# Performance work log

Hardware: AMD Instinct MI355X
Metric: run time of the kernel (lower is better)

## Reference

```python
import jax, jax.numpy as jnp
import numpy as np

NUM_HEADS = 32
HEAD_DIM = 128
NUM_KV_HEADS = 8
SCALE = 0.08838834764831845  # 1/sqrt(128)
T = 2048          # total packed tokens (total_q == total_k in delta branch)
N_SAL = 512       # number of salient rows
NUM_SEQS = 4
EPS = 1e-8
NEG = -1e30


def setup_inputs() -> dict:
    key = jax.random.key(0)
    ks = jax.random.split(key, 5)
    q = jax.random.normal(ks[0], (T, NUM_HEADS, HEAD_DIM), dtype=jnp.float32)
    k = jax.random.normal(ks[1], (T, NUM_KV_HEADS, HEAD_DIM), dtype=jnp.float32)
    v = jax.random.normal(ks[2], (N_SAL, NUM_KV_HEADS, HEAD_DIM), dtype=jnp.float32)
    v_cache = jax.random.normal(ks[3], (T, NUM_KV_HEADS, HEAD_DIM), dtype=jnp.float32)
    c_cache = jax.random.normal(ks[4], (T, NUM_HEADS * HEAD_DIM), dtype=jnp.float32)
    # unique, sorted salient row indices (torch index_copy requires well-defined scatter)
    idx_salient_row = (jnp.arange(N_SAL, dtype=jnp.int64) * (T // N_SAL))
    # 4 equal packed sequences
    cu_seqlens = jnp.array([0, 512, 1024, 1536, 2048], dtype=jnp.int64)
    return {"q": q, "k": k, "v": v, "v_cache": v_cache, "c_cache": c_cache,
            "idx_salient_row": idx_salient_row, "cu_seqlens": cu_seqlens}


def _segment_ids(cu_seqlens, n):
    # seg[i] = which packed sequence row i belongs to (searchsorted right on bounds)
    return jnp.searchsorted(cu_seqlens[1:], jnp.arange(n), side="right")


def _sdpa(q_, k_, v_, seg_q_, seg_k_):
    # GQA: repeat_interleave kv heads to match query heads
    n_rep = q_.shape[1] // k_.shape[1]
    if n_rep > 1:
        k_ = jnp.repeat(k_, n_rep, axis=1)
        v_ = jnp.repeat(v_, n_rep, axis=1)
    scores = jnp.einsum("qhd,khd->hqk", q_, k_) * SCALE  # [H, nq, T]
    allow = (seg_q_[:, None] == seg_k_[None, :])          # [nq, T]
    scores = jnp.where(allow[None, :, :], scores, NEG)
    p = jax.nn.softmax(scores, axis=-1)
    return jnp.einsum("hqk,khd->qhd", p, v_)              # [nq, H, D]


def reference(q, k, v, v_cache, c_cache, idx_salient_row, cu_seqlens):
    total = q.shape[0]
    seg = _segment_ids(cu_seqlens, total)  # seg_q == seg_k (total_q == total_k)

    # delta KV-cache update at salient rows
    v_delta = v - v_cache[idx_salient_row]                      # [n_sal, Hkv, D]
    v_delta_sparse = jnp.zeros_like(k).at[idx_salient_row].set(v_delta)
    v_cache_new = v_cache.at[idx_salient_row].set(v)

    # salient-row full attention against updated cache
    o_salient = _sdpa(q[idx_salient_row], k, v_cache_new, seg[idx_salient_row], seg)
    # sparse delta attention for every row
    delta_c = _sdpa(q, k, v_delta_sparse, seg, seg)

    new_c_flat = c_cache + delta_c.reshape(total, -1)
    new_c_flat = new_c_flat.at[idx_salient_row].set(o_salient.reshape(o_salient.shape[0], -1))

    # cosine similarity between old and new context (early-exit signal)
    num = jnp.sum(c_cache * new_c_flat, axis=-1)
    den_c = jnp.sum(c_cache * c_cache, axis=-1)
    den_n = jnp.sum(new_c_flat * new_c_flat, axis=-1)
    cos_sim = num / (jnp.sqrt(den_c) * jnp.sqrt(den_n) + EPS)

    return new_c_flat.reshape(total, NUM_HEADS, HEAD_DIM), cos_sim
```

## Files before the change

kernel.cpp:

```cpp
#include <hip/hip_runtime.h>
#include <math.h>

#define NUM_HEADS 32
#define HEAD_DIM 128
#define NUM_KV_HEADS 8
#define SCALE 0.08838834764831845f
#define EPS 1e-8f
#define MAX_SEG 512
#define QT 32
#define BLK 512
#define SEGC_MAX 16
#define PB_STRIDE 520
#define TLD 130
#define CD (NUM_HEADS * HEAD_DIM)

typedef __bf16 bf16x8 __attribute__((ext_vector_type(8)));
typedef __bf16 bf16x4 __attribute__((ext_vector_type(4)));
typedef float  f32x4  __attribute__((ext_vector_type(4)));

#define MFMA16(a, b, c) __builtin_amdgcn_mfma_f32_16x16x32_bf16((a), (b), (c), 0, 0, 0)

__device__ __forceinline__ int lower_bound_i(const int* __restrict__ a, int n, int key) {
    int lo = 0, hi = n;
    while (lo < hi) { int mid = (lo + hi) >> 1; if (a[mid] < key) lo = mid + 1; else hi = mid; }
    return lo;
}
__device__ __forceinline__ int bsearch_eq(const int* __restrict__ a, int n, int key) {
    int lo = lower_bound_i(a, n, key);
    return (lo < n && a[lo] == key) ? lo : -1;
}

__device__ __forceinline__ bf16x8 cvt8(const float* p) {
    float4 f0 = *(const float4*)p;
    float4 f1 = *(const float4*)(p + 4);
    bf16x8 a;
    a[0]=(__bf16)f0.x; a[1]=(__bf16)f0.y; a[2]=(__bf16)f0.z; a[3]=(__bf16)f0.w;
    a[4]=(__bf16)f1.x; a[5]=(__bf16)f1.y; a[6]=(__bf16)f1.z; a[7]=(__bf16)f1.w;
    return a;
}

__device__ __forceinline__ void red16(float& xn, float& xc, float& xd) {
#pragma unroll
    for (int m = 1; m <= 8; m <<= 1) {
        xn += __shfl_xor(xn, m, 64);
        xc += __shfl_xor(xc, m, 64);
        xd += __shfl_xor(xd, m, 64);
    }
}

__global__ void prep(const float* __restrict__ k, const float* __restrict__ v,
                     const float* __restrict__ vc, const int* __restrict__ idx,
                     const int* __restrict__ cu,
                     __bf16* __restrict__ kb, __bf16* __restrict__ vnewT,
                     __bf16* __restrict__ vdScat, int* __restrict__ tinfo,
                     int* __restrict__ rowsal,
                     int T, int Tpad, int n_sal, int n_seq,
                     int nb_conv, int nb_vt) {
    __shared__ __bf16 tileN[64 * TLD];
    __shared__ __bf16 tileD[64 * TLD];
    __shared__ int sal_of[64];
    const int b = blockIdx.x;
    const int tid = threadIdx.x;

    if (b < nb_conv) {
        int i = b * 256 + tid;
        int n8 = T * NUM_KV_HEADS * HEAD_DIM / 8;
        if (i < n8) {
            const float4* s4 = (const float4*)(k + (size_t)i * 8);
            float4 a = s4[0], bb = s4[1];
            bf16x8 o;
            o[0]=(__bf16)a.x; o[1]=(__bf16)a.y; o[2]=(__bf16)a.z; o[3]=(__bf16)a.w;
            o[4]=(__bf16)bb.x; o[5]=(__bf16)bb.y; o[6]=(__bf16)bb.z; o[7]=(__bf16)bb.w;
            *(bf16x8*)(kb + (size_t)i * 8) = o;
        }
        return;
    }
    if (b < nb_conv + nb_vt * NUM_KV_HEADS) {
        const int bb = b - nb_conv;
        const int kv = bb / nb_vt;
        const int r0 = (bb % nb_vt) * 64;
        if (tid < 64) sal_of[tid] = bsearch_eq(idx, n_sal, r0 + tid);
        __syncthreads();
        for (int ii = tid; ii < 64 * 32; ii += 256) {
            int r = ii >> 5, c4 = ii & 31;
            int row = r0 + r;
            float4 fN = {0.f, 0.f, 0.f, 0.f};
            float4 fD = {0.f, 0.f, 0.f, 0.f};
            if (row < T) {
                int s2 = sal_of[r];
                if (s2 >= 0) {
                    float4 a  = *(const float4*)(v  + ((size_t)s2  * NUM_KV_HEADS + kv) * HEAD_DIM + c4 * 4);
                    float4 c  = *(const float4*)(vc + ((size_t)row * NUM_KV_HEADS + kv) * HEAD_DIM + c4 * 4);
                    fN = a;
                    fD.x = a.x - c.x; fD.y = a.y - c.y; fD.z = a.z - c.z; fD.w = a.w - c.w;
                } else {
                    fN = *(const float4*)(vc + ((size_t)row * NUM_KV_HEADS + kv) * HEAD_DIM + c4 * 4);
                }
            }
            __bf16* tn = &tileN[r * TLD + c4 * 4];
            tn[0] = (__bf16)fN.x; tn[1] = (__bf16)fN.y; tn[2] = (__bf16)fN.z; tn[3] = (__bf16)fN.w;
            __bf16* td = &tileD[r * TLD + c4 * 4];
            td[0] = (__bf16)fD.x; td[1] = (__bf16)fD.y; td[2] = (__bf16)fD.z; td[3] = (__bf16)fD.w;
        }
        __syncthreads();
        for (int ii = tid; ii < 128 * 8; ii += 256) {
            int d = ii >> 3, rg = ii & 7;
            int row_out = r0 + rg * 8;
            if (row_out < Tpad) {
                bf16x8 oN, oD;
#pragma unroll
                for (int j = 0; j < 8; j++) {
                    oN[j] = tileN[(rg * 8 + j) * TLD + d];
                    oD[j] = tileD[(rg * 8 + j) * TLD + d];
                }
                *(bf16x8*)(vnewT  + ((size_t)kv * HEAD_DIM + d) * Tpad + row_out) = oN;
                *(bf16x8*)(vdScat + ((size_t)kv * HEAD_DIM + d) * Tpad + row_out) = oD;
            }
        }
        return;
    }
    {
        for (int i = tid; i < T; i += 256) rowsal[i] = -1;
        __syncthreads();
        for (int s = tid; s < n_sal; s += 256) rowsal[idx[s]] = s;
        const int NT = T / QT;
        for (int t = tid; t < NT; t += 256) {
            const int r0 = t * QT;
            int a = 0, e = T;
            for (int s = 0; s < n_seq; s++) {
                int x = cu[s], y = cu[s + 1];
                if (r0 >= x && r0 < y) { a = x; e = y; }
            }
            tinfo[t * 4 + 0] = a;
            tinfo[t * 4 + 1] = e;
            tinfo[t * 4 + 2] = 0;
            tinfo[t * 4 + 3] = 0;
        }
    }
}


#define QK_TILE_GEN(ttc) {                                                                  \
    const int t_ = wave * 4 + (ttc);                                                        \
    if (t_ < ntiles) {                                                                      \
        int key_ = seg_start + t_ * 16 + lm;                                                \
        if (key_ >= seg_end) key_ = seg_end - 1;                                            \
        const __bf16* kp_ = kb + ((size_t)key_ * NUM_KV_HEADS + kvh) * HEAD_DIM + quad * 8; \
        const bf16x8 bk0_ = *(const bf16x8*)(kp_);                                          \
        const bf16x8 bk1_ = *(const bf16x8*)(kp_ + 32);                                     \
        const bf16x8 bk2_ = *(const bf16x8*)(kp_ + 64);                                     \
        const bf16x8 bk3_ = *(const bf16x8*)(kp_ + 96);                                     \
        f32x4 a0_ = {0.f,0.f,0.f,0.f}, a1_ = {0.f,0.f,0.f,0.f};                             \
        a0_ = MFMA16(bk0_, aq00, a0_);  a1_ = MFMA16(bk0_, aq10, a1_);                      \
        a0_ = MFMA16(bk1_, aq01, a0_);  a1_ = MFMA16(bk1_, aq11, a1_);                      \
        a0_ = MFMA16(bk2_, aq02, a0_);  a1_ = MFMA16(bk2_, aq12, a1_);                      \
        a0_ = MFMA16(bk3_, aq03, a0_);  a1_ = MFMA16(bk3_, aq13, a1_);                      \
        bf16x4 pk0_, pk1_;                                                                  \
        _Pragma("unroll")                                                                   \
        for (int r_ = 0; r_ < 4; r_++) {                                                    \
            const int kl_ = t_ * 16 + quad * 4 + r_;                                        \
            const bool ok_ = (kl_ < seg_len);                                               \
            float e0_ = ok_ ? __expf(a0_[r_] * SCALE) : 0.f;                                \
            float e1_ = ok_ ? __expf(a1_[r_] * SCALE) : 0.f;                                \
            ps0 += e0_; ps1 += e1_;                                                         \
            pk0_[r_] = (__bf16)e0_; pk1_[r_] = (__bf16)e1_;                                 \
        }                                                                                   \
        *(bf16x4*)&Pb[lm * PB_STRIDE + t_ * 16 + quad * 4] = pk0_;                          \
        *(bf16x4*)&Pb[(16 + lm) * PB_STRIDE + t_ * 16 + quad * 4] = pk1_;                   \
    } }

#define LOADK(buf, t) {                                                                     \
    const __bf16* kn_ = kp + (size_t)(t) * 16 * krow;                                       \
    kk[buf][0] = *(const bf16x8*)(kn_);                                                     \
    kk[buf][1] = *(const bf16x8*)(kn_ + 32);                                                \
    kk[buf][2] = *(const bf16x8*)(kn_ + 64);                                                \
    kk[buf][3] = *(const bf16x8*)(kn_ + 96); }

__global__ __launch_bounds__(BLK, 4)
void attn_mfma(const float* __restrict__ q, const __bf16* __restrict__ kb,
               const __bf16* __restrict__ vnewT, const __bf16* __restrict__ vdScat,
               const float* __restrict__ c_cache, const int* __restrict__ tinfo,
               const int* __restrict__ rowsal,
               float* __restrict__ out_c, float* __restrict__ cospart, int Tpad) {
    const int bid  = blockIdx.x;
    const int kvh  = bid & 7;
    const int rem  = bid >> 3;
    const int h    = kvh * 4 + (rem & 3);
    const int qt   = rem >> 2;
    const int qrow0 = qt * QT;
    const int tid   = threadIdx.x;
    const int wave  = tid >> 6;
    const int lane  = tid & 63;
    const int lm    = lane & 15;
    const int quad  = lane >> 4;

    __shared__ __align__(16) __bf16 Pb[QT * PB_STRIDE];
    __shared__ float wred[8 * QT];
    __shared__ float linv[QT];
    __shared__ int   salrow[QT];
    __shared__ float cp[8 * 3 * QT];

    const int4 ti = *(const int4*)(tinfo + qt * 4);
    const int seg_start = ti.x, seg_end = ti.y;
    const int seg_len = seg_end - seg_start;
    const int ntiles = (seg_len + 15) >> 4;
    const int SEGC   = (seg_len + 31) >> 5;
    const int dim = wave * 16 + lm;

    if (tid < QT) salrow[tid] = rowsal[qrow0 + tid];
    if (ntiles * 16 < SEGC * 32) {
        for (int ii = tid; ii < QT * 16; ii += BLK) {
            int row = ii >> 4, col = ntiles * 16 + (ii & 15);
            Pb[row * PB_STRIDE + col] = (__bf16)0.f;
        }
    }

    bf16x8 aq00, aq01, aq02, aq03, aq10, aq11, aq12, aq13;
    {
        const float* qp0 = q + ((size_t)(qrow0 + lm) * NUM_HEADS + h) * HEAD_DIM + quad * 8;
        const float* qp1 = q + ((size_t)(qrow0 + 16 + lm) * NUM_HEADS + h) * HEAD_DIM + quad * 8;
        aq00 = cvt8(qp0);      aq01 = cvt8(qp0 + 32); aq02 = cvt8(qp0 + 64); aq03 = cvt8(qp0 + 96);
        aq10 = cvt8(qp1);      aq11 = cvt8(qp1 + 32); aq12 = cvt8(qp1 + 64); aq13 = cvt8(qp1 + 96);
    }

    const float* cbase = c_cache + (size_t)qrow0 * CD + h * HEAD_DIM + dim;
    float cold[2][4];
#pragma unroll
    for (int rt = 0; rt < 2; rt++)
#pragma unroll
        for (int r = 0; r < 4; r++)
            cold[rt][r] = cbase[(size_t)(rt * 16 + quad * 4 + r) * CD];

    float ps0 = 0.f, ps1 = 0.f;
    if (seg_len == MAX_SEG) {
        const size_t krow = (size_t)NUM_KV_HEADS * HEAD_DIM;
        const __bf16* kp = kb + (size_t)(seg_start + wave * 64 + lm) * krow
                              + (size_t)kvh * HEAD_DIM + quad * 8;
        bf16x8 kk[3][4];
        LOADK(0, 0)
        LOADK(1, 1)
#pragma unroll
        for (int tt = 0; tt < 4; tt++) {
            if (tt + 2 < 4) LOADK((tt + 2) % 3, tt + 2)
            const int cur = tt % 3;
            f32x4 a0_ = {0.f,0.f,0.f,0.f}, a1_ = {0.f,0.f,0.f,0.f};
            a0_ = MFMA16(kk[cur][0], aq00, a0_);  a1_ = MFMA16(kk[cur][0], aq10, a1_);
            a0_ = MFMA16(kk[cur][1], aq01, a0_);  a1_ = MFMA16(kk[cur][1], aq11, a1_);
            a0_ = MFMA16(kk[cur][2], aq02, a0_);  a1_ = MFMA16(kk[cur][2], aq12, a1_);
            a0_ = MFMA16(kk[cur][3], aq03, a0_);  a1_ = MFMA16(kk[cur][3], aq13, a1_);
            const int t_ = wave * 4 + tt;
            bf16x4 pk0_, pk1_;
#pragma unroll
            for (int r_ = 0; r_ < 4; r_++) {
                float e0_ = __expf(a0_[r_] * SCALE);
                float e1_ = __expf(a1_[r_] * SCALE);
                ps0 += e0_; ps1 += e1_;
                pk0_[r_] = (__bf16)e0_; pk1_[r_] = (__bf16)e1_;
            }
            *(bf16x4*)&Pb[lm * PB_STRIDE + t_ * 16 + quad * 4] = pk0_;
            *(bf16x4*)&Pb[(16 + lm) * PB_STRIDE + t_ * 16 + quad * 4] = pk1_;
        }
    } else {
        QK_TILE_GEN(0) QK_TILE_GEN(1) QK_TILE_GEN(2) QK_TILE_GEN(3)
    }
#pragma unroll
    for (int m = 16; m <= 32; m <<= 1) {
        ps0 += __shfl_xor(ps0, m, 64);
        ps1 += __shfl_xor(ps1, m, 64);
    }
    if (quad == 0) {
        wred[wave * QT + lm]      = ps0;
        wred[wave * QT + 16 + lm] = ps1;
    }

    const __bf16* vF = vnewT  + ((size_t)kvh * HEAD_DIM + dim) * Tpad + seg_start + quad * 8;
    const __bf16* vD = vdScat + ((size_t)kvh * HEAD_DIM + dim) * Tpad + seg_start + quad * 8;
    const __bf16* pb0 = &Pb[lm * PB_STRIDE + quad * 8];
    const __bf16* pb1 = &Pb[(16 + lm) * PB_STRIDE + quad * 8];
    bf16x8 fv[4], dv[4];
#pragma unroll
    for (int i = 0; i < 3; i++) {
        fv[i] = *(const bf16x8*)(vF + i * 32);
        dv[i] = *(const bf16x8*)(vD + i * 32);
    }

    __syncthreads();
    if (tid < QT) {
        float s = 0.f;
#pragma unroll
        for (int w = 0; w < 8; w++) s += wred[w * QT + tid];
        linv[tid] = 1.f / s;
    }

    __builtin_amdgcn_s_setprio(1);
    f32x4 accF0 = {0.f,0.f,0.f,0.f}, accF1 = {0.f,0.f,0.f,0.f};
    f32x4 accD0 = {0.f,0.f,0.f,0.f}, accD1 = {0.f,0.f,0.f,0.f};
    if (SEGC == SEGC_MAX) {
        bf16x8 a0c = *(const bf16x8*)(pb0);
        bf16x8 a1c = *(const bf16x8*)(pb1);
#pragma unroll
        for (int cc = 0; cc < SEGC_MAX; cc++) {
            bf16x8 a0n, a1n;
            if (cc + 1 < SEGC_MAX) {
                a0n = *(const bf16x8*)(pb0 + (cc + 1) * 32);
                a1n = *(const bf16x8*)(pb1 + (cc + 1) * 32);
            }
            if (cc + 3 < SEGC_MAX) {
                fv[(cc + 3) & 3] = *(const bf16x8*)(vF + (cc + 3) * 32);
                dv[(cc + 3) & 3] = *(const bf16x8*)(vD + (cc + 3) * 32);
            }
            const int cur = cc & 3;
            accF0 = MFMA16(a0c, fv[cur], accF0);
            accF1 = MFMA16(a1c, fv[cur], accF1);
            accD0 = MFMA16(a0c, dv[cur], accD0);
            accD1 = MFMA16(a1c, dv[cur], accD1);
            if (cc + 1 < SEGC_MAX) { a0c = a0n; a1c = a1n; }
        }
    } else {
        for (int cc = 0; cc < SEGC; cc++) {
            const bf16x8 bF_ = *(const bf16x8*)(vF + cc * 32);
            const bf16x8 bD_ = *(const bf16x8*)(vD + cc * 32);
            const bf16x8 a0_ = *(const bf16x8*)(pb0 + cc * 32);
            const bf16x8 a1_ = *(const bf16x8*)(pb1 + cc * 32);
            accF0 = MFMA16(a0_, bF_, accF0);
            accF1 = MFMA16(a1_, bF_, accF1);
            accD0 = MFMA16(a0_, bD_, accD0);
            accD1 = MFMA16(a1_, bD_, accD1);
        }
    }
    __builtin_amdgcn_s_setprio(0);
    __syncthreads();

    float* obase = out_c + (size_t)qrow0 * CD + h * HEAD_DIM + dim;
#pragma unroll
    for (int rt = 0; rt < 2; rt++) {
#pragma unroll
        for (int r = 0; r < 4; r++) {
            const int row = rt * 16 + quad * 4 + r;
            const float c_old = cold[rt][r];
            const float li = linv[row];
            const float aF = (rt == 0) ? accF0[r] : accF1[r];
            const float aD = (rt == 0) ? accD0[r] : accD1[r];
            const float o = (salrow[row] >= 0) ? aF * li : c_old + aD * li;
            obase[(size_t)row * CD] = o;
            float xn = o * c_old, xc = c_old * c_old, xd = o * o;
            red16(xn, xc, xd);
            if (lm == 0) {
                cp[(wave * 3 + 0) * QT + row] = xn;
                cp[(wave * 3 + 1) * QT + row] = xc;
                cp[(wave * 3 + 2) * QT + row] = xd;
            }
        }
    }
    __syncthreads();
    for (int ii = tid; ii < 3 * QT; ii += BLK) {
        int c = ii >> 5, row = ii & 31;
        float s = 0.f;
#pragma unroll
        for (int w = 0; w < 8; w++) s += cp[(w * 3 + c) * QT + row];
        cospart[((size_t)(qrow0 + row) * 3 + c) * NUM_HEADS + h] = s;
    }
}

__global__ void cos_finalize(const float* __restrict__ cospart, float* __restrict__ out_cos, int T) {
    const int lane = threadIdx.x & 63;
    const int row  = blockIdx.x * 4 + (threadIdx.x >> 6);
    if (row >= T) return;
    const float* p = cospart + (size_t)row * (NUM_HEADS * 3);
    float a = p[lane];
    float b = (lane < 32) ? p[64 + lane] : 0.f;
#pragma unroll
    for (int m = 1; m <= 16; m <<= 1) {
        a += __shfl_xor(a, m, 64);
        b += __shfl_xor(b, m, 64);
    }
    float den_c = __shfl(a, 32, 64);
    if (lane == 0) out_cos[row] = a / (sqrtf(den_c) * sqrtf(b) + EPS);
}

extern "C" void kernel_launch(void* const* d_in, const int* in_sizes, int n_in,
                              void* d_out, int out_size, void* d_ws, size_t ws_size,
                              hipStream_t stream) {
    const float* q       = (const float*)d_in[0];
    const float* k       = (const float*)d_in[1];
    const float* v       = (const float*)d_in[2];
    const float* v_cache = (const float*)d_in[3];
    const float* c_cache = (const float*)d_in[4];
    const int*   idx     = (const int*)d_in[5];
    const int*   cu      = (const int*)d_in[6];

    const int T     = in_sizes[0] / CD;
    const int n_sal = in_sizes[5];
    const int n_seq = in_sizes[6] - 1;
    const int Tpad  = T + 32;
    const int NT    = T / QT;

    float* out_c   = (float*)d_out;
    float* out_cos = out_c + (size_t)T * CD;

    char* wsp = (char*)d_ws;
    size_t off = 0;
    __bf16* kb = (__bf16*)(wsp + off);
    off += (((size_t)T * NUM_KV_HEADS * HEAD_DIM * 2) + 255) & ~(size_t)255;
    __bf16* vnewT = (__bf16*)(wsp + off);
    off += (((size_t)NUM_KV_HEADS * HEAD_DIM * Tpad * 2) + 255) & ~(size_t)255;
    __bf16* vdScat = (__bf16*)(wsp + off);
    off += (((size_t)NUM_KV_HEADS * HEAD_DIM * Tpad * 2) + 255) & ~(size_t)255;
    float* cospart = (float*)(wsp + off);
    off += ((size_t)T * NUM_HEADS * 3 * 4 + 255) & ~(size_t)255;
    int* tinfo = (int*)(wsp + off);
    off += ((size_t)NT * 4 * 4 + 255) & ~(size_t)255;
    int* rowsal = (int*)(wsp + off);
    off += ((size_t)T * 4 + 255) & ~(size_t)255;
    (void)ws_size;

    const int nb_conv = (T * NUM_KV_HEADS * HEAD_DIM / 8 + 255) / 256;
    const int nb_vt   = (Tpad + 63) / 64;
    const int nb_tot  = nb_conv + nb_vt * NUM_KV_HEADS + 1;

    prep<<<nb_tot, 256, 0, stream>>>(k, v, v_cache, idx, cu, kb, vnewT, vdScat,
                                     tinfo, rowsal, T, Tpad, n_sal, n_seq,
                                     nb_conv, nb_vt);

    attn_mfma<<<NT * NUM_HEADS, BLK, 0, stream>>>(q, kb, vnewT, vdScat, c_cache,
                                                  tinfo, rowsal, out_c, cospart, Tpad);

    cos_finalize<<<(T + 3) / 4, 256, 0, stream>>>(cospart, out_cos, T);
}
```

Before: 227.7 us.

## Process two query heads per block to halve grid size and amortize setup

Each attention block now loops over two query heads that share a KV head, so the grid shrinks from NT*32 to NT*16 blocks. The per-block setup (tile info, salient-row flags, Pb padding) is done once for both heads, and the V tiles may be reused through cache between the two iterations. Cosine partials are accumulated across the two heads in shared memory, and cos_finalize is reworked for the resulting 16-wide partial layout. The cost is fewer blocks, which leaves less parallelism to hide latency, plus the head loop running serially inside each block.

```diff
diff --git a/kernel.cpp b/kernel.cpp
--- a/kernel.cpp
+++ b/kernel.cpp
@@ -184,9 +184,8 @@
                float* __restrict__ out_c, float* __restrict__ cospart, int Tpad) {
     const int bid  = blockIdx.x;
     const int kvh  = bid & 7;
-    const int rem  = bid >> 3;
-    const int h    = kvh * 4 + (rem & 3);
-    const int qt   = rem >> 2;
+    const int sub  = (bid >> 3) & 1;
+    const int qt   = bid >> 4;
     const int qrow0 = qt * QT;
     const int tid   = threadIdx.x;
     const int wave  = tid >> 6;
@@ -215,140 +214,147 @@
         }
     }
 
-    bf16x8 aq00, aq01, aq02, aq03, aq10, aq11, aq12, aq13;
-    {
-        const float* qp0 = q + ((size_t)(qrow0 + lm) * NUM_HEADS + h) * HEAD_DIM + quad * 8;
-        const float* qp1 = q + ((size_t)(qrow0 + 16 + lm) * NUM_HEADS + h) * HEAD_DIM + quad * 8;
-        aq00 = cvt8(qp0);      aq01 = cvt8(qp0 + 32); aq02 = cvt8(qp0 + 64); aq03 = cvt8(qp0 + 96);
-        aq10 = cvt8(qp1);      aq11 = cvt8(qp1 + 32); aq12 = cvt8(qp1 + 64); aq13 = cvt8(qp1 + 96);
-    }
-
-    const float* cbase = c_cache + (size_t)qrow0 * CD + h * HEAD_DIM + dim;
-    float cold[2][4];
-#pragma unroll
-    for (int rt = 0; rt < 2; rt++)
-#pragma unroll
-        for (int r = 0; r < 4; r++)
-            cold[rt][r] = cbase[(size_t)(rt * 16 + quad * 4 + r) * CD];
-
-    float ps0 = 0.f, ps1 = 0.f;
-    if (seg_len == MAX_SEG) {
-        const size_t krow = (size_t)NUM_KV_HEADS * HEAD_DIM;
-        const __bf16* kp = kb + (size_t)(seg_start + wave * 64 + lm) * krow
-                              + (size_t)kvh * HEAD_DIM + quad * 8;
-        bf16x8 kk[3][4];
-        LOADK(0, 0)
-        LOADK(1, 1)
-#pragma unroll
-        for (int tt = 0; tt < 4; tt++) {
-            if (tt + 2 < 4) LOADK((tt + 2) % 3, tt + 2)
-            const int cur = tt % 3;
-            f32x4 a0_ = {0.f,0.f,0.f,0.f}, a1_ = {0.f,0.f,0.f,0.f};
-            a0_ = MFMA16(kk[cur][0], aq00, a0_);  a1_ = MFMA16(kk[cur][0], aq10, a1_);
-            a0_ = MFMA16(kk[cur][1], aq01, a0_);  a1_ = MFMA16(kk[cur][1], aq11, a1_);
-            a0_ = MFMA16(kk[cur][2], aq02, a0_);  a1_ = MFMA16(kk[cur][2], aq12, a1_);
-            a0_ = MFMA16(kk[cur][3], aq03, a0_);  a1_ = MFMA16(kk[cur][3], aq13, a1_);
-            const int t_ = wave * 4 + tt;
-            bf16x4 pk0_, pk1_;
-#pragma unroll
-            for (int r_ = 0; r_ < 4; r_++) {
-                float e0_ = __expf(a0_[r_] * SCALE);
-                float e1_ = __expf(a1_[r_] * SCALE);
-                ps0 += e0_; ps1 += e1_;
-                pk0_[r_] = (__bf16)e0_; pk1_[r_] = (__bf16)e1_;
-            }
-            *(bf16x4*)&Pb[lm * PB_STRIDE + t_ * 16 + quad * 4] = pk0_;
-            *(bf16x4*)&Pb[(16 + lm) * PB_STRIDE + t_ * 16 + quad * 4] = pk1_;
-        }
-    } else {
-        QK_TILE_GEN(0) QK_TILE_GEN(1) QK_TILE_GEN(2) QK_TILE_GEN(3)
-    }
-#pragma unroll
-    for (int m = 16; m <= 32; m <<= 1) {
-        ps0 += __shfl_xor(ps0, m, 64);
-        ps1 += __shfl_xor(ps1, m, 64);
-    }
-    if (quad == 0) {
-        wred[wave * QT + lm]      = ps0;
-        wred[wave * QT + 16 + lm] = ps1;
-    }
-
     const __bf16* vF = vnewT  + ((size_t)kvh * HEAD_DIM + dim) * Tpad + seg_start + quad * 8;
     const __bf16* vD = vdScat + ((size_t)kvh * HEAD_DIM + dim) * Tpad + seg_start + quad * 8;
     const __bf16* pb0 = &Pb[lm * PB_STRIDE + quad * 8];
     const __bf16* pb1 = &Pb[(16 + lm) * PB_STRIDE + quad * 8];
-    bf16x8 fv[4], dv[4];
-#pragma unroll
-    for (int i = 0; i < 3; i++) {
-        fv[i] = *(const bf16x8*)(vF + i * 32);
-        dv[i] = *(const bf16x8*)(vD + i * 32);
-    }
-
-    __syncthreads();
-    if (tid < QT) {
-        float s = 0.f;
-#pragma unroll
-        for (int w = 0; w < 8; w++) s += wred[w * QT + tid];
-        linv[tid] = 1.f / s;
-    }
-
-    __builtin_amdgcn_s_setprio(1);
-    f32x4 accF0 = {0.f,0.f,0.f,0.f}, accF1 = {0.f,0.f,0.f,0.f};
-    f32x4 accD0 = {0.f,0.f,0.f,0.f}, accD1 = {0.f,0.f,0.f,0.f};
-    if (SEGC == SEGC_MAX) {
-        bf16x8 a0c = *(const bf16x8*)(pb0);
-        bf16x8 a1c = *(const bf16x8*)(pb1);
-#pragma unroll
-        for (int cc = 0; cc < SEGC_MAX; cc++) {
-            bf16x8 a0n, a1n;
-            if (cc + 1 < SEGC_MAX) {
-                a0n = *(const bf16x8*)(pb0 + (cc + 1) * 32);
-                a1n = *(const bf16x8*)(pb1 + (cc + 1) * 32);
-            }
-            if (cc + 3 < SEGC_MAX) {
-                fv[(cc + 3) & 3] = *(const bf16x8*)(vF + (cc + 3) * 32);
-                dv[(cc + 3) & 3] = *(const bf16x8*)(vD + (cc + 3) * 32);
-            }
-            const int cur = cc & 3;
-            accF0 = MFMA16(a0c, fv[cur], accF0);
-            accF1 = MFMA16(a1c, fv[cur], accF1);
-            accD0 = MFMA16(a0c, dv[cur], accD0);
-            accD1 = MFMA16(a1c, dv[cur], accD1);
-            if (cc + 1 < SEGC_MAX) { a0c = a0n; a1c = a1n; }
-        }
-    } else {
-        for (int cc = 0; cc < SEGC; cc++) {
-            const bf16x8 bF_ = *(const bf16x8*)(vF + cc * 32);
-            const bf16x8 bD_ = *(const bf16x8*)(vD + cc * 32);
-            const bf16x8 a0_ = *(const bf16x8*)(pb0 + cc * 32);
-            const bf16x8 a1_ = *(const bf16x8*)(pb1 + cc * 32);
-            accF0 = MFMA16(a0_, bF_, accF0);
-            accF1 = MFMA16(a1_, bF_, accF1);
-            accD0 = MFMA16(a0_, bD_, accD0);
-            accD1 = MFMA16(a1_, bD_, accD1);
-        }
-    }
-    __builtin_amdgcn_s_setprio(0);
-    __syncthreads();
-
-    float* obase = out_c + (size_t)qrow0 * CD + h * HEAD_DIM + dim;
-#pragma unroll
-    for (int rt = 0; rt < 2; rt++) {
-#pragma unroll
-        for (int r = 0; r < 4; r++) {
-            const int row = rt * 16 + quad * 4 + r;
-            const float c_old = cold[rt][r];
-            const float li = linv[row];
-            const float aF = (rt == 0) ? accF0[r] : accF1[r];
-            const float aD = (rt == 0) ? accD0[r] : accD1[r];
-            const float o = (salrow[row] >= 0) ? aF * li : c_old + aD * li;
-            obase[(size_t)row * CD] = o;
-            float xn = o * c_old, xc = c_old * c_old, xd = o * o;
-            red16(xn, xc, xd);
-            if (lm == 0) {
-                cp[(wave * 3 + 0) * QT + row] = xn;
-                cp[(wave * 3 + 1) * QT + row] = xc;
-                cp[(wave * 3 + 2) * QT + row] = xd;
+
+#pragma unroll 1
+    for (int u = 0; u < 2; u++) {
+        const int h = kvh * 4 + sub * 2 + u;
+
+        bf16x8 aq00, aq01, aq02, aq03, aq10, aq11, aq12, aq13;
+        {
+            const float* qp0 = q + ((size_t)(qrow0 + lm) * NUM_HEADS + h) * HEAD_DIM + quad * 8;
+            const float* qp1 = q + ((size_t)(qrow0 + 16 + lm) * NUM_HEADS + h) * HEAD_DIM + quad * 8;
+            aq00 = cvt8(qp0);      aq01 = cvt8(qp0 + 32); aq02 = cvt8(qp0 + 64); aq03 = cvt8(qp0 + 96);
+            aq10 = cvt8(qp1);      aq11 = cvt8(qp1 + 32); aq12 = cvt8(qp1 + 64); aq13 = cvt8(qp1 + 96);
+        }
+        const float* cbase = c_cache + (size_t)qrow0 * CD + h * HEAD_DIM + dim;
+        float cold[2][4];
+#pragma unroll
+        for (int rt = 0; rt < 2; rt++)
+#pragma unroll
+            for (int r = 0; r < 4; r++)
+                cold[rt][r] = cbase[(size_t)(rt * 16 + quad * 4 + r) * CD];
+
+        float ps0 = 0.f, ps1 = 0.f;
+        if (seg_len == MAX_SEG) {
+            const size_t krow = (size_t)NUM_KV_HEADS * HEAD_DIM;
+            const __bf16* kp = kb + (size_t)(seg_start + wave * 64 + lm) * krow
+                                  + (size_t)kvh * HEAD_DIM + quad * 8;
+            bf16x8 kk[3][4];
+            LOADK(0, 0)
+            LOADK(1, 1)
+#pragma unroll
+            for (int tt = 0; tt < 4; tt++) {
+                if (tt + 2 < 4) LOADK((tt + 2) % 3, tt + 2)
+                const int cur = tt % 3;
+                f32x4 a0_ = {0.f,0.f,0.f,0.f}, a1_ = {0.f,0.f,0.f,0.f};
+                a0_ = MFMA16(kk[cur][0], aq00, a0_);  a1_ = MFMA16(kk[cur][0], aq10, a1_);
+                a0_ = MFMA16(kk[cur][1], aq01, a0_);  a1_ = MFMA16(kk[cur][1], aq11, a1_);
+                a0_ = MFMA16(kk[cur][2], aq02, a0_);  a1_ = MFMA16(kk[cur][2], aq12, a1_);
+                a0_ = MFMA16(kk[cur][3], aq03, a0_);  a1_ = MFMA16(kk[cur][3], aq13, a1_);
+                const int t_ = wave * 4 + tt;
+                bf16x4 pk0_, pk1_;
+#pragma unroll
+                for (int r_ = 0; r_ < 4; r_++) {
+                    float e0_ = __expf(a0_[r_] * SCALE);
+                    float e1_ = __expf(a1_[r_] * SCALE);
+                    ps0 += e0_; ps1 += e1_;
+                    pk0_[r_] = (__bf16)e0_; pk1_[r_] = (__bf16)e1_;
+                }
+                *(bf16x4*)&Pb[lm * PB_STRIDE + t_ * 16 + quad * 4] = pk0_;
+                *(bf16x4*)&Pb[(16 + lm) * PB_STRIDE + t_ * 16 + quad * 4] = pk1_;
+            }
+        } else {
+            QK_TILE_GEN(0) QK_TILE_GEN(1) QK_TILE_GEN(2) QK_TILE_GEN(3)
+        }
+#pragma unroll
+        for (int m = 16; m <= 32; m <<= 1) {
+            ps0 += __shfl_xor(ps0, m, 64);
+            ps1 += __shfl_xor(ps1, m, 64);
+        }
+        if (quad == 0) {
+            wred[wave * QT + lm]      = ps0;
+            wred[wave * QT + 16 + lm] = ps1;
+        }
+
+        bf16x8 fv[4], dv[4];
+#pragma unroll
+        for (int i = 0; i < 3; i++) {
+            fv[i] = *(const bf16x8*)(vF + i * 32);
+            dv[i] = *(const bf16x8*)(vD + i * 32);
+        }
+
+        __syncthreads();
+        if (tid < QT) {
+            float s = 0.f;
+#pragma unroll
+            for (int w = 0; w < 8; w++) s += wred[w * QT + tid];
+            linv[tid] = 1.f / s;
+        }
+
+        __builtin_amdgcn_s_setprio(1);
+        f32x4 accF0 = {0.f,0.f,0.f,0.f}, accF1 = {0.f,0.f,0.f,0.f};
+        f32x4 accD0 = {0.f,0.f,0.f,0.f}, accD1 = {0.f,0.f,0.f,0.f};
+        if (SEGC == SEGC_MAX) {
+            bf16x8 a0c = *(const bf16x8*)(pb0);
+            bf16x8 a1c = *(const bf16x8*)(pb1);
+#pragma unroll
+            for (int cc = 0; cc < SEGC_MAX; cc++) {
+                bf16x8 a0n, a1n;
+                if (cc + 1 < SEGC_MAX) {
+                    a0n = *(const bf16x8*)(pb0 + (cc + 1) * 32);
+                    a1n = *(const bf16x8*)(pb1 + (cc + 1) * 32);
+                }
+                if (cc + 3 < SEGC_MAX) {
+                    fv[(cc + 3) & 3] = *(const bf16x8*)(vF + (cc + 3) * 32);
+                    dv[(cc + 3) & 3] = *(const bf16x8*)(vD + (cc + 3) * 32);
+                }
+                const int cur = cc & 3;
+                accF0 = MFMA16(a0c, fv[cur], accF0);
+                accF1 = MFMA16(a1c, fv[cur], accF1);
+                accD0 = MFMA16(a0c, dv[cur], accD0);
+                accD1 = MFMA16(a1c, dv[cur], accD1);
+                if (cc + 1 < SEGC_MAX) { a0c = a0n; a1c = a1n; }
+            }
+        } else {
+            for (int cc = 0; cc < SEGC; cc++) {
+                const bf16x8 bF_ = *(const bf16x8*)(vF + cc * 32);
+                const bf16x8 bD_ = *(const bf16x8*)(vD + cc * 32);
+                const bf16x8 a0_ = *(const bf16x8*)(pb0 + cc * 32);
+                const bf16x8 a1_ = *(const bf16x8*)(pb1 + cc * 32);
+                accF0 = MFMA16(a0_, bF_, accF0);
+                accF1 = MFMA16(a1_, bF_, accF1);
+                accD0 = MFMA16(a0_, bD_, accD0);
+                accD1 = MFMA16(a1_, bD_, accD1);
+            }
+        }
+        __builtin_amdgcn_s_setprio(0);
+        __syncthreads();
+
+        float* obase = out_c + (size_t)qrow0 * CD + h * HEAD_DIM + dim;
+#pragma unroll
+        for (int rt = 0; rt < 2; rt++) {
+#pragma unroll
+            for (int r = 0; r < 4; r++) {
+                const int row = rt * 16 + quad * 4 + r;
+                const float c_old = cold[rt][r];
+                const float li = linv[row];
+                const float aF = (rt == 0) ? accF0[r] : accF1[r];
+                const float aD = (rt == 0) ? accD0[r] : accD1[r];
+                const float o = (salrow[row] >= 0) ? aF * li : c_old + aD * li;
+                obase[(size_t)row * CD] = o;
+                float xn = o * c_old, xc = c_old * c_old, xd = o * o;
+                red16(xn, xc, xd);
+                if (lm == 0) {
+                    const int s0 = (wave * 3 + 0) * QT + row;
+                    const int s1 = (wave * 3 + 1) * QT + row;
+                    const int s2 = (wave * 3 + 2) * QT + row;
+                    if (u == 0) { cp[s0] = xn;  cp[s1] = xc;  cp[s2] = xd; }
+                    else        { cp[s0] += xn; cp[s1] += xc; cp[s2] += xd; }
+                }
             }
         }
     }
@@ -358,7 +364,7 @@
         float s = 0.f;
 #pragma unroll
         for (int w = 0; w < 8; w++) s += cp[(w * 3 + c) * QT + row];
-        cospart[((size_t)(qrow0 + row) * 3 + c) * NUM_HEADS + h] = s;
+        cospart[(size_t)(qrow0 + row) * 48 + c * 16 + kvh * 2 + sub] = s;
     }
 }
 
@@ -366,16 +372,16 @@
     const int lane = threadIdx.x & 63;
     const int row  = blockIdx.x * 4 + (threadIdx.x >> 6);
     if (row >= T) return;
-    const float* p = cospart + (size_t)row * (NUM_HEADS * 3);
-    float a = p[lane];
-    float b = (lane < 32) ? p[64 + lane] : 0.f;
-#pragma unroll
-    for (int m = 1; m <= 16; m <<= 1) {
-        a += __shfl_xor(a, m, 64);
-        b += __shfl_xor(b, m, 64);
-    }
-    float den_c = __shfl(a, 32, 64);
-    if (lane == 0) out_cos[row] = a / (sqrtf(den_c) * sqrtf(b) + EPS);
+    const float* p = cospart + (size_t)row * 48;
+    float vv = (lane < 48) ? p[lane] : 0.f;
+    vv += __shfl_xor(vv, 1, 64);
+    vv += __shfl_xor(vv, 2, 64);
+    vv += __shfl_xor(vv, 4, 64);
+    vv += __shfl_xor(vv, 8, 64);
+    const float nn = __shfl(vv, 0, 64);
+    const float dc = __shfl(vv, 16, 64);
+    const float dd = __shfl(vv, 32, 64);
+    if (lane == 0) out_cos[row] = nn / (sqrtf(dc) * sqrtf(dd) + EPS);
 }
 
 extern "C" void kernel_launch(void* const* d_in, const int* in_sizes, int n_in,
@@ -407,7 +413,7 @@
     __bf16* vdScat = (__bf16*)(wsp + off);
     off += (((size_t)NUM_KV_HEADS * HEAD_DIM * Tpad * 2) + 255) & ~(size_t)255;
     float* cospart = (float*)(wsp + off);
-    off += ((size_t)T * NUM_HEADS * 3 * 4 + 255) & ~(size_t)255;
+    off += ((size_t)T * 48 * 4 + 255) & ~(size_t)255;
     int* tinfo = (int*)(wsp + off);
     off += ((size_t)NT * 4 * 4 + 255) & ~(size_t)255;
     int* rowsal = (int*)(wsp + off);
@@ -422,8 +428,8 @@
                                      tinfo, rowsal, T, Tpad, n_sal, n_seq,
                                      nb_conv, nb_vt);
 
-    attn_mfma<<<NT * NUM_HEADS, BLK, 0, stream>>>(q, kb, vnewT, vdScat, c_cache,
-                                                  tinfo, rowsal, out_c, cospart, Tpad);
+    attn_mfma<<<NT * 16, BLK, 0, stream>>>(q, kb, vnewT, vdScat, c_cache,
+                                           tinfo, rowsal, out_c, cospart, Tpad);
 
     cos_finalize<<<(T + 3) / 4, 256, 0, stream>>>(cospart, out_cos, T);
 }
```

New measurement: 311.6 us. 36.9% more time.

## Compact delta attention to salient columns only in PV matmul

Applied to the files above, without the earlier changes.

Adds a compacted, transposed v_delta buffer holding only the salient rows, plus per-tile salient index ranges. The attention kernel scatters the probabilities of salient keys into a small Pd shared tile and runs the delta PV matmul over only those columns, instead of multiplying against the mostly zero dense scattered V delta. This removes about three quarters of the delta MFMAs and V loads. It costs extra shared memory, per-key rowsal lookups during softmax, and extra prep blocks.

```diff
diff --git a/kernel.cpp b/kernel.cpp
--- a/kernel.cpp
+++ b/kernel.cpp
@@ -11,6 +11,10 @@
 #define BLK 512
 #define SEGC_MAX 16
 #define PB_STRIDE 520
+#define PD_STRIDE 136
+#define PD_MAX 128
+#define SAL_PAD 576
+#define SAL_STRIDE 640
 #define TLD 130
 #define CD (NUM_HEADS * HEAD_DIM)
 
@@ -52,10 +56,10 @@
                      const float* __restrict__ vc, const int* __restrict__ idx,
                      const int* __restrict__ cu,
                      __bf16* __restrict__ kb, __bf16* __restrict__ vnewT,
-                     __bf16* __restrict__ vdScat, int* __restrict__ tinfo,
-                     int* __restrict__ rowsal,
+                     __bf16* __restrict__ vdScat, __bf16* __restrict__ vdT,
+                     int* __restrict__ tinfo, int* __restrict__ rowsal,
                      int T, int Tpad, int n_sal, int n_seq,
-                     int nb_conv, int nb_vt) {
+                     int nb_conv, int nb_vt, int nb_vd) {
     __shared__ __bf16 tileN[64 * TLD];
     __shared__ __bf16 tileD[64 * TLD];
     __shared__ int sal_of[64];
@@ -119,6 +123,33 @@
         }
         return;
     }
+    if (b < nb_conv + nb_vt * NUM_KV_HEADS + nb_vd * NUM_KV_HEADS) {
+        const int bb = b - nb_conv - nb_vt * NUM_KV_HEADS;
+        const int kv = bb / nb_vd;
+        const int s0 = (bb % nb_vd) * 64;
+        for (int ii = tid; ii < 64 * 32; ii += 256) {
+            int r = ii >> 5, c4 = ii & 31;
+            int s = s0 + r;
+            float4 f = {0.f, 0.f, 0.f, 0.f};
+            if (s < n_sal) {
+                int row = idx[s];
+                float4 a  = *(const float4*)(v  + ((size_t)s   * NUM_KV_HEADS + kv) * HEAD_DIM + c4 * 4);
+                float4 c2 = *(const float4*)(vc + ((size_t)row * NUM_KV_HEADS + kv) * HEAD_DIM + c4 * 4);
+                f.x = a.x - c2.x; f.y = a.y - c2.y; f.z = a.z - c2.z; f.w = a.w - c2.w;
+            }
+            __bf16* tp = &tileN[r * TLD + c4 * 4];
+            tp[0] = (__bf16)f.x; tp[1] = (__bf16)f.y; tp[2] = (__bf16)f.z; tp[3] = (__bf16)f.w;
+        }
+        __syncthreads();
+        for (int ii = tid; ii < 128 * 8; ii += 256) {
+            int d = ii >> 3, rg = ii & 7;
+            bf16x8 o;
+#pragma unroll
+            for (int j = 0; j < 8; j++) o[j] = tileN[(rg * 8 + j) * TLD + d];
+            *(bf16x8*)(vdT + ((size_t)kv * HEAD_DIM + d) * SAL_STRIDE + s0 + rg * 8) = o;
+        }
+        return;
+    }
     {
         for (int i = tid; i < T; i += 256) rowsal[i] = -1;
         __syncthreads();
@@ -133,8 +164,8 @@
             }
             tinfo[t * 4 + 0] = a;
             tinfo[t * 4 + 1] = e;
-            tinfo[t * 4 + 2] = 0;
-            tinfo[t * 4 + 3] = 0;
+            tinfo[t * 4 + 2] = lower_bound_i(idx, n_sal, a);
+            tinfo[t * 4 + 3] = lower_bound_i(idx, n_sal, e);
         }
     }
 }
@@ -164,6 +195,14 @@
             float e1_ = ok_ ? __expf(a1_[r_] * SCALE) : 0.f;                                \
             ps0 += e0_; ps1 += e1_;                                                         \
             pk0_[r_] = (__bf16)e0_; pk1_[r_] = (__bf16)e1_;                                 \
+            if (compact && ok_) {                                                           \
+                int sr_ = rowsal[seg_start + kl_];                                          \
+                if (sr_ >= 0) {                                                             \
+                    int c_ = sr_ - s_lo;                                                    \
+                    Pd[lm * PD_STRIDE + c_]        = pk0_[r_];                              \
+                    Pd[(16 + lm) * PD_STRIDE + c_] = pk1_[r_];                              \
+                }                                                                           \
+            }                                                                               \
         }                                                                                   \
         *(bf16x4*)&Pb[lm * PB_STRIDE + t_ * 16 + quad * 4] = pk0_;                          \
         *(bf16x4*)&Pb[(16 + lm) * PB_STRIDE + t_ * 16 + quad * 4] = pk1_;                   \
@@ -179,9 +218,11 @@
 __global__ __launch_bounds__(BLK, 4)
 void attn_mfma(const float* __restrict__ q, const __bf16* __restrict__ kb,
                const __bf16* __restrict__ vnewT, const __bf16* __restrict__ vdScat,
+               const __bf16* __restrict__ vdT,
                const float* __restrict__ c_cache, const int* __restrict__ tinfo,
                const int* __restrict__ rowsal,
-               float* __restrict__ out_c, float* __restrict__ cospart, int Tpad) {
+               float* __restrict__ out_c, float* __restrict__ cospart,
+               int Tpad, int use_compact) {
     const int bid  = blockIdx.x;
     const int kvh  = bid & 7;
     const int rem  = bid >> 3;
@@ -195,17 +236,20 @@
     const int quad  = lane >> 4;
 
     __shared__ __align__(16) __bf16 Pb[QT * PB_STRIDE];
+    __shared__ __align__(16) __bf16 Pd[QT * PD_STRIDE];
     __shared__ float wred[8 * QT];
     __shared__ float linv[QT];
     __shared__ int   salrow[QT];
     __shared__ float cp[8 * 3 * QT];
 
     const int4 ti = *(const int4*)(tinfo + qt * 4);
-    const int seg_start = ti.x, seg_end = ti.y;
+    const int seg_start = ti.x, seg_end = ti.y, s_lo = ti.z, s_hi = ti.w;
     const int seg_len = seg_end - seg_start;
+    const int nss    = s_hi - s_lo;
     const int ntiles = (seg_len + 15) >> 4;
     const int SEGC   = (seg_len + 31) >> 5;
     const int dim = wave * 16 + lm;
+    const bool compact = use_compact && (nss <= PD_MAX);
 
     if (tid < QT) salrow[tid] = rowsal[qrow0 + tid];
     if (ntiles * 16 < SEGC * 32) {
@@ -213,6 +257,11 @@
             int row = ii >> 4, col = ntiles * 16 + (ii & 15);
             Pb[row * PB_STRIDE + col] = (__bf16)0.f;
         }
+    }
+    if (compact) {
+        const bf16x8 z = {0,0,0,0,0,0,0,0};
+        for (int ii = tid; ii < QT * PD_STRIDE / 8; ii += BLK)
+            ((bf16x8*)Pd)[ii] = z;
     }
 
     bf16x8 aq00, aq01, aq02, aq03, aq10, aq11, aq12, aq13;
@@ -259,6 +308,18 @@
             }
             *(bf16x4*)&Pb[lm * PB_STRIDE + t_ * 16 + quad * 4] = pk0_;
             *(bf16x4*)&Pb[(16 + lm) * PB_STRIDE + t_ * 16 + quad * 4] = pk1_;
+            if (compact) {
+                const int4 sal4 = *(const int4*)&rowsal[seg_start + t_ * 16 + quad * 4];
+                const int srl[4] = {sal4.x, sal4.y, sal4.z, sal4.w};
+#pragma unroll
+                for (int r_ = 0; r_ < 4; r_++) {
+                    if (srl[r_] >= 0) {
+                        const int c_ = srl[r_] - s_lo;
+                        Pd[lm * PD_STRIDE + c_]        = pk0_[r_];
+                        Pd[(16 + lm) * PD_STRIDE + c_] = pk1_[r_];
+                    }
+                }
+            }
         }
     } else {
         QK_TILE_GEN(0) QK_TILE_GEN(1) QK_TILE_GEN(2) QK_TILE_GEN(3)
@@ -281,7 +342,7 @@
 #pragma unroll
     for (int i = 0; i < 3; i++) {
         fv[i] = *(const bf16x8*)(vF + i * 32);
-        dv[i] = *(const bf16x8*)(vD + i * 32);
+        if (!compact) dv[i] = *(const bf16x8*)(vD + i * 32);
     }
 
     __syncthreads();
@@ -295,37 +356,79 @@
     __builtin_amdgcn_s_setprio(1);
     f32x4 accF0 = {0.f,0.f,0.f,0.f}, accF1 = {0.f,0.f,0.f,0.f};
     f32x4 accD0 = {0.f,0.f,0.f,0.f}, accD1 = {0.f,0.f,0.f,0.f};
-    if (SEGC == SEGC_MAX) {
-        bf16x8 a0c = *(const bf16x8*)(pb0);
-        bf16x8 a1c = *(const bf16x8*)(pb1);
-#pragma unroll
-        for (int cc = 0; cc < SEGC_MAX; cc++) {
-            bf16x8 a0n, a1n;
-            if (cc + 1 < SEGC_MAX) {
-                a0n = *(const bf16x8*)(pb0 + (cc + 1) * 32);
-                a1n = *(const bf16x8*)(pb1 + (cc + 1) * 32);
-            }
-            if (cc + 3 < SEGC_MAX) {
-                fv[(cc + 3) & 3] = *(const bf16x8*)(vF + (cc + 3) * 32);
-                dv[(cc + 3) & 3] = *(const bf16x8*)(vD + (cc + 3) * 32);
-            }
-            const int cur = cc & 3;
-            accF0 = MFMA16(a0c, fv[cur], accF0);
-            accF1 = MFMA16(a1c, fv[cur], accF1);
-            accD0 = MFMA16(a0c, dv[cur], accD0);
-            accD1 = MFMA16(a1c, dv[cur], accD1);
-            if (cc + 1 < SEGC_MAX) { a0c = a0n; a1c = a1n; }
+    if (compact) {
+        const int ndc = (nss + 31) >> 5;
+        const __bf16* vdb = vdT + ((size_t)kvh * HEAD_DIM + dim) * SAL_STRIDE + s_lo + quad * 8;
+        const bool al8 = ((s_lo & 7) == 0);
+        for (int dc = 0; dc < ndc; dc++) {
+            bf16x8 bvD;
+            const __bf16* vp = vdb + dc * 32;
+            if (al8) bvD = *(const bf16x8*)vp;
+            else {
+#pragma unroll
+                for (int j = 0; j < 8; j++) bvD[j] = vp[j];
+            }
+            const bf16x8 aD0 = *(const bf16x8*)&Pd[lm * PD_STRIDE + dc * 32 + quad * 8];
+            const bf16x8 aD1 = *(const bf16x8*)&Pd[(16 + lm) * PD_STRIDE + dc * 32 + quad * 8];
+            accD0 = MFMA16(aD0, bvD, accD0);
+            accD1 = MFMA16(aD1, bvD, accD1);
+        }
+        if (SEGC == SEGC_MAX) {
+            bf16x8 a0c = *(const bf16x8*)(pb0);
+            bf16x8 a1c = *(const bf16x8*)(pb1);
+#pragma unroll
+            for (int cc = 0; cc < SEGC_MAX; cc++) {
+                bf16x8 a0n, a1n;
+                if (cc + 1 < SEGC_MAX) {
+                    a0n = *(const bf16x8*)(pb0 + (cc + 1) * 32);
+                    a1n = *(const bf16x8*)(pb1 + (cc + 1) * 32);
+                }
+                if (cc + 3 < SEGC_MAX)
+                    fv[(cc + 3) & 3] = *(const bf16x8*)(vF + (cc + 3) * 32);
+                accF0 = MFMA16(a0c, fv[cc & 3], accF0);
+                accF1 = MFMA16(a1c, fv[cc & 3], accF1);
+                if (cc + 1 < SEGC_MAX) { a0c = a0n; a1c = a1n; }
+            }
+        } else {
+            for (int cc = 0; cc < SEGC; cc++) {
+                const bf16x8 bF_ = *(const bf16x8*)(vF + cc * 32);
+                accF0 = MFMA16(*(const bf16x8*)(pb0 + cc * 32), bF_, accF0);
+                accF1 = MFMA16(*(const bf16x8*)(pb1 + cc * 32), bF_, accF1);
+            }
         }
     } else {
-        for (int cc = 0; cc < SEGC; cc++) {
-            const bf16x8 bF_ = *(const bf16x8*)(vF + cc * 32);
-            const bf16x8 bD_ = *(const bf16x8*)(vD + cc * 32);
-            const bf16x8 a0_ = *(const bf16x8*)(pb0 + cc * 32);
-            const bf16x8 a1_ = *(const bf16x8*)(pb1 + cc * 32);
-            accF0 = MFMA16(a0_, bF_, accF0);
-            accF1 = MFMA16(a1_, bF_, accF1);
-            accD0 = MFMA16(a0_, bD_, accD0);
-            accD1 = MFMA16(a1_, bD_, accD1);
+        if (SEGC == SEGC_MAX) {
+            bf16x8 a0c = *(const bf16x8*)(pb0);
+            bf16x8 a1c = *(const bf16x8*)(pb1);
+#pragma unroll
+            for (int cc = 0; cc < SEGC_MAX; cc++) {
+                bf16x8 a0n, a1n;
+                if (cc + 1 < SEGC_MAX) {
+                    a0n = *(const bf16x8*)(pb0 + (cc + 1) * 32);
+                    a1n = *(const bf16x8*)(pb1 + (cc + 1) * 32);
+                }
+                if (cc + 3 < SEGC_MAX) {
+                    fv[(cc + 3) & 3] = *(const bf16x8*)(vF + (cc + 3) * 32);
+                    dv[(cc + 3) & 3] = *(const bf16x8*)(vD + (cc + 3) * 32);
+                }
+                const int cur = cc & 3;
+                accF0 = MFMA16(a0c, fv[cur], accF0);
+                accF1 = MFMA16(a1c, fv[cur], accF1);
+                accD0 = MFMA16(a0c, dv[cur], accD0);
+                accD1 = MFMA16(a1c, dv[cur], accD1);
+                if (cc + 1 < SEGC_MAX) { a0c = a0n; a1c = a1n; }
+            }
+        } else {
+            for (int cc = 0; cc < SEGC; cc++) {
+                const bf16x8 bF_ = *(const bf16x8*)(vF + cc * 32);
+                const bf16x8 bD_ = *(const bf16x8*)(vD + cc * 32);
+                const bf16x8 a0_ = *(const bf16x8*)(pb0 + cc * 32);
+                const bf16x8 a1_ = *(const bf16x8*)(pb1 + cc * 32);
+                accF0 = MFMA16(a0_, bF_, accF0);
+                accF1 = MFMA16(a1_, bF_, accF1);
+                accD0 = MFMA16(a0_, bD_, accD0);
+                accD1 = MFMA16(a1_, bD_, accD1);
+            }
         }
     }
     __builtin_amdgcn_s_setprio(0);
@@ -394,6 +497,7 @@
     const int n_seq = in_sizes[6] - 1;
     const int Tpad  = T + 32;
     const int NT    = T / QT;
+    const int use_compact = (n_sal <= SAL_PAD) ? 1 : 0;
 
     float* out_c   = (float*)d_out;
     float* out_cos = out_c + (size_t)T * CD;
@@ -406,6 +510,8 @@
     off += (((size_t)NUM_KV_HEADS * HEAD_DIM * Tpad * 2) + 255) & ~(size_t)255;
     __bf16* vdScat = (__bf16*)(wsp + off);
     off += (((size_t)NUM_KV_HEADS * HEAD_DIM * Tpad * 2) + 255) & ~(size_t)255;
+    __bf16* vdT = (__bf16*)(wsp + off);
+    off += (((size_t)NUM_KV_HEADS * HEAD_DIM * SAL_STRIDE * 2) + 255) & ~(size_t)255;
     float* cospart = (float*)(wsp + off);
     off += ((size_t)T * NUM_HEADS * 3 * 4 + 255) & ~(size_t)255;
     int* tinfo = (int*)(wsp + off);
@@ -416,14 +522,16 @@
 
     const int nb_conv = (T * NUM_KV_HEADS * HEAD_DIM / 8 + 255) / 256;
     const int nb_vt   = (Tpad + 63) / 64;
-    const int nb_tot  = nb_conv + nb_vt * NUM_KV_HEADS + 1;
-
-    prep<<<nb_tot, 256, 0, stream>>>(k, v, v_cache, idx, cu, kb, vnewT, vdScat,
+    const int nb_vd   = use_compact ? (SAL_STRIDE / 64) : 0;
+    const int nb_tot  = nb_conv + nb_vt * NUM_KV_HEADS + nb_vd * NUM_KV_HEADS + 1;
+
+    prep<<<nb_tot, 256, 0, stream>>>(k, v, v_cache, idx, cu, kb, vnewT, vdScat, vdT,
                                      tinfo, rowsal, T, Tpad, n_sal, n_seq,
-                                     nb_conv, nb_vt);
-
-    attn_mfma<<<NT * NUM_HEADS, BLK, 0, stream>>>(q, kb, vnewT, vdScat, c_cache,
-                                                  tinfo, rowsal, out_c, cospart, Tpad);
+                                     nb_conv, nb_vt, nb_vd);
+
+    attn_mfma<<<NT * NUM_HEADS, BLK, 0, stream>>>(q, kb, vnewT, vdScat, vdT, c_cache,
+                                                  tinfo, rowsal, out_c, cospart,
+                                                  Tpad, use_compact);
 
     cos_finalize<<<(T + 3) / 4, 256, 0, stream>>>(cospart, out_cos, T);
 }
```

Measured after the change: 225.7 us. Within noise of the previous version (-0.9%).
